# Performance work log

Measured on AMD Instinct MI355X. Metric: run time of the kernel, lower is better.

## Reference

```python
import jax, jax.numpy as jnp
import numpy as np

CONF_T = 0.6   # default conf_threshold
IOU_T = 0.5    # default iou_threshold
ALPHA = 0.25
GAMMA = 2.0


def _nms_np(boxes, scores, iou_t):
    """Greedy NMS (torchvision semantics: keep while IoU <= iou_t), returns kept indices
    into `boxes`, sorted by decreasing score. Pure numpy; data-dependent output size."""
    order = np.argsort(-scores, kind="stable")
    b = boxes[order]
    x1, y1, x2, y2 = b[:, 0], b[:, 1], b[:, 2], b[:, 3]
    areas = (x2 - x1) * (y2 - y1)
    M = b.shape[0]
    suppressed = np.zeros(M, dtype=bool)
    keep = []
    for i in range(M):
        if suppressed[i]:
            continue
        keep.append(order[i])
        if i + 1 >= M:
            break
        xx1 = np.maximum(x1[i], x1[i + 1:]); yy1 = np.maximum(y1[i], y1[i + 1:])
        xx2 = np.minimum(x2[i], x2[i + 1:]); yy2 = np.minimum(y2[i], y2[i + 1:])
        inter = np.clip(xx2 - xx1, 0, None) * np.clip(yy2 - yy1, 0, None)
        iou = inter / (areas[i] + areas[i + 1:] - inter)
        suppressed[i + 1:] |= iou > iou_t
    return np.asarray(keep, dtype=np.int64)


def _select_indices(loc, conf):
    """Concrete (non-traced) confidence filtering + NMS; index selection is
    non-differentiable in the original torch code as well."""
    conf_np = np.asarray(conf)
    if conf_np.ndim == 3:
        conf_np = conf_np[0]                      # conf.squeeze(0)
    scores = conf_np.max(axis=1)                  # conf.max(dim=1)
    filt_idx = np.nonzero(scores > CONF_T)[0]     # mask filter
    boxes = np.asarray(loc)[0, filt_idx]          # loc[:, mask, :].squeeze(0)
    nms_score = conf_np[filt_idx, 0]              # score = filtered_conf[:, 0]
    nms_keep = _nms_np(boxes, nms_score, IOU_T)
    return filt_idx, nms_keep


def _smooth_l1_sum(pred, target):
    # SmoothL1Loss(beta=1.0, reduction='sum'); target (k,4) broadcasts against
    # pred (k,C,4) exactly as torch does (requires C == k).
    d = jnp.abs(pred - target)
    return jnp.sum(jnp.where(d < 1.0, 0.5 * d * d, d - 0.5))


def _loss(loc, conf, target_boxes, target_labels_f, filt_idx, nms_keep, k):
    conf2 = conf[0] if conf.ndim == 3 else conf   # (N,C)
    floc = loc[0, filt_idx]                       # (M,4) filtered boxes
    fconf = conf2[filt_idx]                       # (M,C)
    mloc = floc[nms_keep]                         # (P,4) NMS-kept boxes
    mconf = fconf[nms_keep]                       # (P,C)
    # torch.topk(matched_conf, k, dim=0): per-class column top-k
    vals, idx = jax.lax.top_k(mconf.T, k)         # (C,k) each
    vals, idx = vals.T, idx.T                     # (k,C)
    conf_bin = (vals[:, 0] > 0.5).astype(jnp.float32)   # (k,) hard 0/1 "logits"
    pred_box = mloc[idx]                          # (k,C,4) gather, as matched_loc[indices,:]
    loc_loss = _smooth_l1_sum(pred_box, target_boxes)
    # F.cross_entropy with 1-D input and float target => soft-label CE (scalar)
    ce = -jnp.sum(target_labels_f * jax.nn.log_softmax(conf_bin))
    p_t = jnp.exp(-ce)
    conf_loss = ALPHA * (1.0 - p_t) ** GAMMA * ce
    num_pos = jnp.asarray(nms_keep.shape[0], dtype=jnp.float32)
    return (loc_loss + conf_loss) / num_pos


def setup_inputs() -> dict:
    key = jax.random.key(0)
    k0, k1, k2, k3 = jax.random.split(key, 4)
    N, C, K = 8192, 20, 20
    return {
        "loc": jax.random.uniform(k0, (1, N, 4), dtype=jnp.float32),
        "conf": jax.random.uniform(k1, (1, N, C), dtype=jnp.float32),
        "target_boxes": jax.random.uniform(k2, (K, 4), dtype=jnp.float32),
        "target_labels": jax.random.randint(k3, (K,), 0, C).astype(jnp.int64),
    }


def reference(loc, conf, target_boxes, target_labels):
    filt_idx, nms_keep = _select_indices(loc, conf)
    if filt_idx.size == 0 or nms_keep.size == 0:
        return jnp.float32(0.001)
    k = int(target_labels.shape[0])
    return _loss(loc, conf, target_boxes,
                 target_labels.astype(jnp.float32),
                 jnp.asarray(filt_idx), jnp.asarray(nms_keep), k)
```

## Files before the change

### kernel.cpp

```cpp
#include <hip/hip_runtime.h>
#include <stdint.h>
#include <stddef.h>


#define NCAP 8192
#define WROW (NCAP / 64)

typedef unsigned long long u64;

constexpr size_t OFF_CNT   = 0;
constexpr size_t OFF_KEYS  = 256;
constexpr size_t OFF_SX1   = OFF_KEYS + 8ull * NCAP;
constexpr size_t OFF_SY1   = OFF_SX1 + 4ull * NCAP;
constexpr size_t OFF_SX2   = OFF_SY1 + 4ull * NCAP;
constexpr size_t OFF_SY2   = OFF_SX2 + 4ull * NCAP;
constexpr size_t OFF_AREA  = OFF_SY2 + 4ull * NCAP;
constexpr size_t OFF_SORIG = OFF_AREA + 4ull * NCAP;
constexpr size_t OFF_KEEPS = OFF_SORIG + 4ull * NCAP;
constexpr size_t OFF_KORIG = OFF_KEEPS + 4ull * NCAP;
constexpr size_t OFF_TOPV  = OFF_KORIG + 4ull * NCAP;
constexpr size_t OFF_TOPI  = OFF_TOPV + 4096;
constexpr size_t OFF_DIAG2 = OFF_TOPI + 4096;
constexpr size_t OFF_MASK  = OFF_DIAG2 + 16ull * NCAP;
constexpr size_t WS_NEED_MASK = OFF_MASK + 8ull * NCAP * WROW;

__device__ __forceinline__ void barrier_nodrain() {
  asm volatile("s_waitcnt lgkmcnt(0)" ::: "memory");
  __builtin_amdgcn_s_barrier();
  asm volatile("" ::: "memory");
}

template <int CTRL, int RMASK>
__device__ __forceinline__ unsigned or_dpp_step(unsigned x) {
  return x | (unsigned)__builtin_amdgcn_update_dpp(0, (int)x, CTRL, RMASK, 0xf, true);
}
__device__ __forceinline__ u64 wave_or64(u64 x) {
  unsigned lo = (unsigned)x, hi = (unsigned)(x >> 32);
  lo = or_dpp_step<0x111, 0xf>(lo); hi = or_dpp_step<0x111, 0xf>(hi);
  lo = or_dpp_step<0x112, 0xf>(lo); hi = or_dpp_step<0x112, 0xf>(hi);
  lo = or_dpp_step<0x114, 0xf>(lo); hi = or_dpp_step<0x114, 0xf>(hi);
  lo = or_dpp_step<0x118, 0xf>(lo); hi = or_dpp_step<0x118, 0xf>(hi);
  lo = or_dpp_step<0x142, 0xa>(lo); hi = or_dpp_step<0x142, 0xa>(hi);
  lo = or_dpp_step<0x143, 0xc>(lo); hi = or_dpp_step<0x143, 0xc>(hi);
  lo = (unsigned)__builtin_amdgcn_readlane((int)lo, 63);
  hi = (unsigned)__builtin_amdgcn_readlane((int)hi, 63);
  return ((u64)hi << 32) | lo;
}

#define SS1(M)                                                              \
  { int tt = base + (M) * 64 + l;                                           \
    u64 a = e[M];                                                           \
    unsigned slo = __shfl_xor((unsigned)a, (int)jj);                        \
    unsigned shi = __shfl_xor((unsigned)(a >> 32), (int)jj);                \
    u64 b = ((u64)shi << 32) | slo;                                         \
    bool up = ((tt & bk) == 0);                                             \
    bool lowr = ((l & (int)jj) == 0);                                       \
    bool tmin = (up == lowr);                                               \
    bool agtb = (a > b);                                                    \
    e[M] = (tmin == agtb) ? b : a; }

#define SSTEP() { SS1(0) SS1(1) SS1(2) SS1(3) SS1(4) SS1(5) SS1(6) SS1(7) }

#define CSW(A, B)                                                           \
  { int tt = base + (A) * 64 + l;                                           \
    bool up = ((tt & bk) == 0);                                             \
    u64 xa = e[A], xb = e[B];                                               \
    bool sw = up ? (xa > xb) : (xa < xb);                                   \
    e[A] = sw ? xb : xa; e[B] = sw ? xa : xb; }

#define RSTEP4() { CSW(0,4) CSW(1,5) CSW(2,6) CSW(3,7) }
#define RSTEP2() { CSW(0,2) CSW(1,3) CSW(4,6) CSW(5,7) }
#define RSTEP1() { CSW(0,1) CSW(2,3) CSW(4,5) CSW(6,7) }

__global__ __launch_bounds__(64) void k_psort(
    const float* __restrict__ conf, int N, int C,
    u64* __restrict__ keys) {
  const int l = threadIdx.x;
  const int base = blockIdx.x * 512;
  const bool vec4 = ((C & 3) == 0);
  u64 e[8];
#pragma unroll
  for (int m = 0; m < 8; ++m) {
    int row = base + m * 64 + l;
    u64 key;
    if (row < N) {
      const float* cr = conf + (size_t)row * C;
      float mx, c0;
      if (vec4) {
        const float4* cr4 = (const float4*)cr;
        float4 q = cr4[0];
        c0 = q.x;
        mx = fmaxf(fmaxf(q.x, q.y), fmaxf(q.z, q.w));
        for (int k = 1; k < (C >> 2); ++k) {
          float4 p = cr4[k];
          mx = fmaxf(mx, fmaxf(fmaxf(p.x, p.y), fmaxf(p.z, p.w)));
        }
      } else {
        c0 = cr[0];
        mx = c0;
        for (int c = 1; c < C; ++c) mx = fmaxf(mx, cr[c]);
      }
      unsigned int k32;
      if (mx > 0.6f) {
        union { float f; unsigned int u; } s; s.f = c0;
        unsigned int u = s.u;
        u = (u & 0x80000000u) ? ~u : (u | 0x80000000u);
        k32 = ~u;
        if (k32 == 0xFFFFFFFFu) k32 = 0xFFFFFFFEu;
      } else {
        k32 = 0xFFFFFFFFu;
      }
      key = ((u64)k32 << 32) | (unsigned int)row;
    } else {
      key = ((u64)0xFFFFFFFFu << 32);
    }
    e[m] = key;
  }
  for (unsigned bk = 2; bk <= 512; bk <<= 1) {
    unsigned j = bk >> 1;
    if (j == 256) { RSTEP4(); j = 128; }
    if (j == 128) { RSTEP2(); j = 64; }
    if (j == 64)  { RSTEP1(); j = 32; }
    for (unsigned jj = j; jj >= 1; jj >>= 1) SSTEP();
  }
#pragma unroll
  for (int m = 0; m < 8; ++m) keys[base + m * 64 + l] = e[m];
}

__global__ __launch_bounds__(1024) void k_merge(
    const float* __restrict__ loc,
    u64* __restrict__ keys, unsigned int* __restrict__ cnt,
    float* __restrict__ sx1, float* __restrict__ sy1,
    float* __restrict__ sx2, float* __restrict__ sy2,
    float* __restrict__ sarea, unsigned int* __restrict__ sorig) {
  __shared__ u64 sk[NCAP];
  __shared__ int wsum[16];
  const int tid = threadIdx.x;
  const int w = tid >> 6, l = tid & 63;
  const int base = w * 512;
  u64 e[8];
#pragma unroll
  for (int m = 0; m < 8; ++m) e[m] = keys[base + m * 64 + l];

  for (unsigned bk = 1024; bk <= NCAP; bk <<= 1) {
    unsigned j = bk >> 1;
    {
#pragma unroll
      for (int m = 0; m < 8; ++m) sk[base + m * 64 + l] = e[m];
      __syncthreads();
      for (unsigned j2 = bk >> 1; j2 >= 512; j2 >>= 1) {
        for (int tl = tid; tl < NCAP; tl += 1024) {
          unsigned p = (unsigned)tl ^ j2;
          if (p > (unsigned)tl) {
            bool up = ((tl & bk) == 0);
            u64 x = sk[tl], y = sk[p];
            bool sw = up ? (x > y) : (x < y);
            if (sw) { sk[tl] = y; sk[p] = x; }
          }
        }
        __syncthreads();
      }
#pragma unroll
      for (int m = 0; m < 8; ++m) e[m] = sk[base + m * 64 + l];
      __syncthreads();
      j = 256;
    }
    if (j == 256) { RSTEP4(); j = 128; }
    if (j == 128) { RSTEP2(); j = 64; }
    if (j == 64)  { RSTEP1(); j = 32; }
    for (unsigned jj = j; jj >= 1; jj >>= 1) SSTEP();
  }

  int cv = 0;
#pragma unroll
  for (int m = 0; m < 8; ++m) {
    int idx = base + m * 64 + l;
    u64 key = e[m];
    if ((key >> 32) != 0xFFFFFFFFull) ++cv;
    unsigned row = (unsigned)(key & 0xFFFFFFFFull);
    float4 b4 = *(const float4*)(loc + (size_t)row * 4);
    float x1 = b4.x, y1 = b4.y, x2 = b4.z, y2 = b4.w;
    sx1[idx] = x1; sy1[idx] = y1; sx2[idx] = x2; sy2[idx] = y2;
    sarea[idx] = (x2 - x1) * (y2 - y1);
    sorig[idx] = row;
  }
  for (int off = 32; off; off >>= 1) cv += __shfl_down(cv, off);
  if (l == 0) wsum[w] = cv;
  __syncthreads();
  if (tid == 0) {
    int s = 0;
    for (int i = 0; i < 16; ++i) s += wsum[i];
    cnt[0] = (unsigned int)s;
  }
}

__global__ __launch_bounds__(64) void k_mask(
    const float* __restrict__ sx1, const float* __restrict__ sy1,
    const float* __restrict__ sx2, const float* __restrict__ sy2,
    const float* __restrict__ sarea,
    u64* __restrict__ mask, u64* __restrict__ diagI) {
  if (blockIdx.y < (blockIdx.x & ~1u)) return;
  __shared__ float jx1[64], jy1[64], jx2[64], jy2[64], ja[64];
  int t = threadIdx.x;
  int jbase = blockIdx.y * 64;
  jx1[t] = sx1[jbase + t]; jy1[t] = sy1[jbase + t];
  jx2[t] = sx2[jbase + t]; jy2[t] = sy2[jbase + t];
  ja[t]  = sarea[jbase + t];
  __syncthreads();
  int i = blockIdx.x * 64 + t;
  float xi1 = sx1[i], yi1 = sy1[i], xi2 = sx2[i], yi2 = sy2[i], ai = sarea[i];
  u64 bits = 0ULL;
#pragma unroll 8
  for (int jj = 0; jj < 64; ++jj) {
    float xx1 = fmaxf(xi1, jx1[jj]);
    float yy1 = fmaxf(yi1, jy1[jj]);
    float xx2 = fminf(xi2, jx2[jj]);
    float yy2 = fminf(yi2, jy2[jj]);
    float w = fmaxf(xx2 - xx1, 0.0f);
    float h = fmaxf(yy2 - yy1, 0.0f);
    float inter = w * h;
    float den = ai + ja[jj] - inter;
    float iou = inter / den;
    if (iou > 0.5f) bits |= (1ULL << jj);
  }
  mask[(size_t)i * WROW + blockIdx.y] = bits;
  if ((blockIdx.y >> 1) == (blockIdx.x >> 1))
    diagI[((size_t)i << 1) + (blockIdx.y & 1)] = bits;
}

__global__ __launch_bounds__(1024) void k_scan(
    const u64* __restrict__ mask,
    const u64* __restrict__ diagIg,
    unsigned int* __restrict__ cnt,
    unsigned int* __restrict__ keeps) {
  __shared__ __align__(16) u64 ldsDiag[2 * NCAP];
  __shared__ __align__(16) u64 rem[WROW];
  __shared__ u64 ldsKA, ldsKB;
  __shared__ int ldsKb;
  const int tid = threadIdx.x;
  const int F = (int)cnt[0];
  const int nch = (F + 127) >> 7;
  const ulonglong2* __restrict__ m2 = (const ulonglong2*)mask;

  for (int i = tid; i < 2 * NCAP; i += 1024) ldsDiag[i] = diagIg[i];
  for (int w = tid; w < WROW; w += 1024) rem[w] = 0;

  const int p0 = tid & 63;
  const int g0 = tid >> 6;
  int K = 0;
  __syncthreads();

  for (int H = 0; H < nch; ++H) {
    const size_t gb = (size_t)H * 8192;
    const int base = H << 7;
    const bool ld = (p0 > H);
    ulonglong2 v0 = {0,0}, v1 = {0,0}, v2 = {0,0}, v3 = {0,0},
               v4 = {0,0}, v5 = {0,0}, v6 = {0,0}, v7 = {0,0};
    if (ld) {
      v0 = m2[gb + tid];
      v1 = m2[gb + tid + 1024];
      v2 = m2[gb + tid + 2048];
      v3 = m2[gb + tid + 3072];
      v4 = m2[gb + tid + 4096];
      v5 = m2[gb + tid + 5120];
      v6 = m2[gb + tid + 6144];
      v7 = m2[gb + tid + 7168];
    }
    barrier_nodrain();

    if (tid < 64) {
      ulonglong2 dAB = *(const ulonglong2*)&ldsDiag[(size_t)(base + tid) << 1];
      u64 DA = dAB.x, AB = dAB.y;
      u64 DB = ldsDiag[(((size_t)(base + 64 + tid)) << 1) + 1];
      ulonglong2 supP = *(const ulonglong2*)&rem[2 * H];
      u64 sup0 = supP.x, supB0 = supP.y;

      int remrows = F - base;
      u64 validA = (remrows >= 64) ? ~0ull : ((1ull << remrows) - 1ull);
      int r2 = remrows - 64;
      u64 validB = (r2 >= 64) ? ~0ull : ((r2 <= 0) ? 0ull : ((1ull << r2) - 1ull));

      u64 DfwdA = (tid < 63) ? (DA & (~0ull << (tid + 1))) : 0ull;
      u64 undec = validA & ~sup0;
      u64 dmask = ((undec >> tid) & 1ull) ? DfwdA : 0ull;
      u64 vuln = wave_or64(dmask);
      u64 dang = __ballot(dmask != 0ull);
      u64 involved = (dang | vuln) & undec;
      u64 keepA = undec & ~involved;
      u64 und2 = involved;
      {
        unsigned Flo = (unsigned)DfwdA, Fhi = (unsigned)(DfwdA >> 32);
        while (und2) {
          int rr = __builtin_ctzll(und2);
          keepA |= 1ull << rr;
          unsigned dlo = __builtin_amdgcn_readlane(Flo, rr);
          unsigned dhi = __builtin_amdgcn_readlane(Fhi, rr);
          und2 &= ~((((u64)dhi << 32) | (u64)dlo) | (1ull << rr));
        }
      }

      u64 abm = ((keepA >> tid) & 1ull) ? AB : 0ull;
      u64 supB = supB0 | wave_or64(abm);
      u64 DfwdB = (tid < 63) ? (DB & (~0ull << (tid + 1))) : 0ull;
      u64 undecB = validB & ~supB;
      u64 dmaskB = ((undecB >> tid) & 1ull) ? DfwdB : 0ull;
      u64 vulnB = wave_or64(dmaskB);
      u64 dangB = __ballot(dmaskB != 0ull);
      u64 involvedB = (dangB | vulnB) & undecB;
      u64 keepB = undecB & ~involvedB;
      u64 und2B = involvedB;
      {
        unsigned Flo = (unsigned)DfwdB, Fhi = (unsigned)(DfwdB >> 32);
        while (und2B) {
          int rr = __builtin_ctzll(und2B);
          keepB |= 1ull << rr;
          unsigned dlo = __builtin_amdgcn_readlane(Flo, rr);
          unsigned dhi = __builtin_amdgcn_readlane(Fhi, rr);
          und2B &= ~((((u64)dhi << 32) | (u64)dlo) | (1ull << rr));
        }
      }

      if (tid == 0) { ldsKA = keepA; ldsKB = keepB; ldsKb = K; }
      K += __popcll(keepA) + __popcll(keepB);
    }
    barrier_nodrain();

    const u64 keepA = ldsKA, keepB = ldsKB;

    if (g0 == 1) {
      const int l = p0;
      const int Kb = ldsKb;
      int pcA = __popcll(keepA);
      unsigned kloA = (unsigned)keepA, khiA = (unsigned)(keepA >> 32);
      int preA = __builtin_amdgcn_mbcnt_hi(khiA, __builtin_amdgcn_mbcnt_lo(kloA, 0));
      if ((keepA >> l) & 1ull) keeps[Kb + preA] = (unsigned)(base + l);
      unsigned kloB = (unsigned)keepB, khiB = (unsigned)(keepB >> 32);
      int preB = __builtin_amdgcn_mbcnt_hi(khiB, __builtin_amdgcn_mbcnt_lo(kloB, 0));
      if ((keepB >> l) & 1ull) keeps[Kb + pcA + preB] = (unsigned)(base + 64 + l);
    }

    if (ld && (keepA | keepB)) {
      u64 ax = 0, ay = 0;
      if ((keepA >> g0) & 1ull)        { ax |= v0.x; ay |= v0.y; }
      if ((keepA >> (g0+16)) & 1ull)   { ax |= v1.x; ay |= v1.y; }
      if ((keepA >> (g0+32)) & 1ull)   { ax |= v2.x; ay |= v2.y; }
      if ((keepA >> (g0+48)) & 1ull)   { ax |= v3.x; ay |= v3.y; }
      if ((keepB >> g0) & 1ull)        { ax |= v4.x; ay |= v4.y; }
      if ((keepB >> (g0+16)) & 1ull)   { ax |= v5.x; ay |= v5.y; }
      if ((keepB >> (g0+32)) & 1ull)   { ax |= v6.x; ay |= v6.y; }
      if ((keepB >> (g0+48)) & 1ull)   { ax |= v7.x; ay |= v7.y; }
      const int w0 = 2 * p0;
      if (ax) atomicOr(&rem[w0], ax);
      if (ay) atomicOr(&rem[w0 + 1], ay);
    }
  }
  if (tid == 0) cnt[1] = (unsigned int)K;
}

__global__ __launch_bounds__(256) void k_scan_nomask(
    const float* __restrict__ sx1, const float* __restrict__ sy1,
    const float* __restrict__ sx2, const float* __restrict__ sy2,
    const float* __restrict__ sarea,
    unsigned int* __restrict__ cnt,
    unsigned int* __restrict__ keeps) {
  __shared__ unsigned char sup[NCAP];
  __shared__ int sK;
  int tid = threadIdx.x;
  int F = (int)cnt[0];
  for (int j = tid; j < NCAP; j += 256) sup[j] = 0;
  if (tid == 0) sK = 0;
  __syncthreads();
  for (int i = 0; i < F; ++i) {
    if (!sup[i]) {
      if (tid == 0) keeps[sK++] = (unsigned int)i;
      float xi1 = sx1[i], yi1 = sy1[i], xi2 = sx2[i], yi2 = sy2[i], ai = sarea[i];
      for (int j = i + 1 + tid; j < F; j += 256) {
        if (sup[j]) continue;
        float xx1 = fmaxf(xi1, sx1[j]);
        float yy1 = fmaxf(yi1, sy1[j]);
        float xx2 = fminf(xi2, sx2[j]);
        float yy2 = fminf(yi2, sy2[j]);
        float w = fmaxf(xx2 - xx1, 0.0f);
        float h = fmaxf(yy2 - yy1, 0.0f);
        float inter = w * h;
        float iou = inter / (ai + sarea[j] - inter);
        if (iou > 0.5f) sup[j] = 1;
      }
    }
    __syncthreads();
  }
  if (tid == 0) cnt[1] = (unsigned int)sK;
}

__global__ __launch_bounds__(1024) void k_topk(
    const float* __restrict__ conf,
    const unsigned int* __restrict__ sorig,
    const unsigned int* __restrict__ keeps,
    const unsigned int* __restrict__ cnt,
    int C, int KT,
    float* __restrict__ topv, int* __restrict__ topi) {
  __shared__ float wlv[16];
  __shared__ int wli[16];
  __shared__ float ldsWv;
  __shared__ int ldsWj;
  const int tid = threadIdx.x;
  const int lane = tid & 63;
  const int wv_ = tid >> 6;
  const int c = blockIdx.x;
  const int M = (int)cnt[1];

  const float NEG = -3.402823466e+38f;
  float v[8];
#pragma unroll
  for (int k = 0; k < 8; ++k) {
    int j = tid + (k << 10);
    v[k] = (j < M) ? conf[(size_t)sorig[keeps[j]] * C + c] : NEG;
  }
  float bv = NEG; int bk_ = -1;
#pragma unroll
  for (int k = 0; k < 8; ++k)
    if (v[k] > bv) { bv = v[k]; bk_ = k; }
  int bj = (bk_ >= 0) ? (tid + (bk_ << 10)) : 0x7FFFFFFF;
  if (bv == NEG) bj = 0x7FFFFFFF;

  for (int t = 0; t < KT; ++t) {
    float rv = bv; int rj = bj;
#pragma unroll
    for (int off = 32; off; off >>= 1) {
      float v2 = __shfl_down(rv, off);
      int   j2 = __shfl_down(rj, off);
      if (v2 > rv || (v2 == rv && j2 < rj)) { rv = v2; rj = j2; }
    }
    if (lane == 0) { wlv[wv_] = rv; wli[wv_] = rj; }
    __syncthreads();
    if (wv_ == 0) {
      float fv = (lane < 16) ? wlv[lane] : NEG;
      int   fj = (lane < 16) ? wli[lane] : 0x7FFFFFFF;
#pragma unroll
      for (int off = 32; off; off >>= 1) {
        float v2 = __shfl_down(fv, off);
        int   j2 = __shfl_down(fj, off);
        if (v2 > fv || (v2 == fv && j2 < fj)) { fv = v2; fj = j2; }
      }
      if (lane == 0) {
        ldsWv = fv; ldsWj = fj;
        topv[c * KT + t] = fv;
        topi[c * KT + t] = (fj == 0x7FFFFFFF) ? 0 : fj;
      }
    }
    __syncthreads();
    const int wj = ldsWj;
    if (wj != 0x7FFFFFFF && (wj & 1023) == tid) {
      int kk = wj >> 10;
#pragma unroll
      for (int k = 0; k < 8; ++k)
        if (k == kk) v[k] = NEG;
      bv = NEG; bk_ = -1;
#pragma unroll
      for (int k = 0; k < 8; ++k)
        if (v[k] > bv) { bv = v[k]; bk_ = k; }
      bj = (bk_ >= 0) ? (tid + (bk_ << 10)) : 0x7FFFFFFF;
      if (bv == NEG) bj = 0x7FFFFFFF;
    }
  }
}

__global__ __launch_bounds__(256) void k_loss(
    const float* __restrict__ loc, const float* __restrict__ tb,
    const int* __restrict__ labels,
    const unsigned int* __restrict__ sorig,
    const unsigned int* __restrict__ keeps,
    const float* __restrict__ topv, const int* __restrict__ topi,
    const unsigned int* __restrict__ cnt, int C, int KT,
    float* __restrict__ out) {
  __shared__ float red[256];
  int tid = threadIdx.x;
  int F = (int)cnt[0];
  int M = (int)cnt[1];
  if (F == 0 || M == 0) {
    if (tid == 0) out[0] = 0.001f;
    return;
  }
  int total = KT * C * 4;
  float part = 0.0f;
  for (int e = tid; e < total; e += 256) {
    int d = e & 3;
    int q = e >> 2;
    int c = q % C;
    int i = q / C;
    int j = topi[c * KT + i];
    unsigned int orow = sorig[keeps[j]];
    float pred = loc[(size_t)orow * 4 + d];
    float tg = tb[c * 4 + d];
    float dd = fabsf(pred - tg);
    part += (dd < 1.0f) ? (0.5f * dd * dd) : (dd - 0.5f);
  }
  red[tid] = part;
  __syncthreads();
  for (int s = 128; s > 0; s >>= 1) {
    if (tid < s) red[tid] += red[tid + s];
    __syncthreads();
  }
  if (tid == 0) {
    float loc_loss = red[0];
    float mx = -3.402823466e+38f;
    for (int i = 0; i < KT; ++i) {
      float x = (topv[i] > 0.5f) ? 1.0f : 0.0f;
      mx = fmaxf(mx, x);
    }
    float ssum = 0.0f;
    for (int i = 0; i < KT; ++i) {
      float x = (topv[i] > 0.5f) ? 1.0f : 0.0f;
      ssum += expf(x - mx);
    }
    float lse = mx + logf(ssum);
    float ce = 0.0f;
    for (int i = 0; i < KT; ++i) {
      float x = (topv[i] > 0.5f) ? 1.0f : 0.0f;
      ce += (float)labels[i] * (x - lse);
    }
    ce = -ce;
    float pt = expf(-ce);
    float om = 1.0f - pt;
    float conf_loss = 0.25f * om * om * ce;
    out[0] = (loc_loss + conf_loss) / (float)M;
  }
}


extern "C" void kernel_launch(void* const* d_in, const int* in_sizes, int n_in,
                              void* d_out, int out_size, void* d_ws, size_t ws_size,
                              hipStream_t stream) {
  (void)n_in; (void)out_size;
  const float* loc    = (const float*)d_in[0];
  const float* conf   = (const float*)d_in[1];
  const float* tb     = (const float*)d_in[2];
  const int*   labels = (const int*)d_in[3];
  float* out = (float*)d_out;

  int N = in_sizes[0] / 4;
  if (N > NCAP) N = NCAP;
  int C  = (N > 0) ? (in_sizes[1] / N) : 20;
  int KT = in_sizes[3];

  char* ws = (char*)d_ws;
  unsigned int* cnt   = (unsigned int*)(ws + OFF_CNT);
  u64*          keys  = (u64*)(ws + OFF_KEYS);
  float*        sx1   = (float*)(ws + OFF_SX1);
  float*        sy1   = (float*)(ws + OFF_SY1);
  float*        sx2   = (float*)(ws + OFF_SX2);
  float*        sy2   = (float*)(ws + OFF_SY2);
  float*        sarea = (float*)(ws + OFF_AREA);
  unsigned int* sorig = (unsigned int*)(ws + OFF_SORIG);
  unsigned int* keeps = (unsigned int*)(ws + OFF_KEEPS);
  float*        topv  = (float*)(ws + OFF_TOPV);
  int*          topi  = (int*)(ws + OFF_TOPI);
  u64*          diagI = (u64*)(ws + OFF_DIAG2);
  u64*          mask  = (u64*)(ws + OFF_MASK);

  bool use_mask = (ws_size >= WS_NEED_MASK);

  k_psort<<<16, 64, 0, stream>>>(conf, N, C, keys);
  k_merge<<<1, 1024, 0, stream>>>(loc, keys, cnt,
                                  sx1, sy1, sx2, sy2, sarea, sorig);
  if (use_mask) {
    k_mask<<<dim3(WROW, WROW), 64, 0, stream>>>(sx1, sy1, sx2, sy2, sarea,
                                                mask, diagI);
    k_scan<<<1, 1024, 0, stream>>>(mask, diagI, cnt, keeps);
  } else {
    k_scan_nomask<<<1, 256, 0, stream>>>(sx1, sy1, sx2, sy2, sarea, cnt, keeps);
  }
  k_topk<<<C, 1024, 0, stream>>>(conf, sorig, keeps, cnt, C, KT, topv, topi);
  k_loss<<<1, 256, 0, stream>>>(loc, tb, labels, sorig, keeps, topv, topi, cnt, C, KT, out);
}
```

Baseline: 300.0 us.

## Prefetch next mask chunk in scan and fuse loss into top-k kernel

The NMS scan kernel now issues the global loads for chunk H+1 before processing chunk H, using double-buffered registers so memory latency overlaps the serial per-chunk decision work. Separately, the loss kernel is folded into the top-k kernel through a last-block-done pattern: each block atomically increments a counter (reset in the merge kernel), and the final block computes the loss. This removes one kernel launch at the cost of extra register pressure in the scan and an atomic plus threadfence in top-k.

```diff
diff --git a/kernel.cpp b/kernel.cpp
--- a/kernel.cpp
+++ b/kernel.cpp
@@ -191,6 +191,7 @@
     int s = 0;
     for (int i = 0; i < 16; ++i) s += wsum[i];
     cnt[0] = (unsigned int)s;
+    cnt[2] = 0u;
   }
 }
 
@@ -248,23 +249,36 @@
   const int p0 = tid & 63;
   const int g0 = tid >> 6;
   int K = 0;
+
+  ulonglong2 v0 = {0,0}, v1 = {0,0}, v2 = {0,0}, v3 = {0,0},
+             v4 = {0,0}, v5 = {0,0}, v6 = {0,0}, v7 = {0,0};
+  if (nch > 0 && p0 > 0) {
+    v0 = m2[tid];
+    v1 = m2[tid + 1024];
+    v2 = m2[tid + 2048];
+    v3 = m2[tid + 3072];
+    v4 = m2[tid + 4096];
+    v5 = m2[tid + 5120];
+    v6 = m2[tid + 6144];
+    v7 = m2[tid + 7168];
+  }
   __syncthreads();
 
   for (int H = 0; H < nch; ++H) {
-    const size_t gb = (size_t)H * 8192;
     const int base = H << 7;
     const bool ld = (p0 > H);
-    ulonglong2 v0 = {0,0}, v1 = {0,0}, v2 = {0,0}, v3 = {0,0},
-               v4 = {0,0}, v5 = {0,0}, v6 = {0,0}, v7 = {0,0};
-    if (ld) {
-      v0 = m2[gb + tid];
-      v1 = m2[gb + tid + 1024];
-      v2 = m2[gb + tid + 2048];
-      v3 = m2[gb + tid + 3072];
-      v4 = m2[gb + tid + 4096];
-      v5 = m2[gb + tid + 5120];
-      v6 = m2[gb + tid + 6144];
-      v7 = m2[gb + tid + 7168];
+    ulonglong2 n0 = {0,0}, n1 = {0,0}, n2 = {0,0}, n3 = {0,0},
+               n4 = {0,0}, n5 = {0,0}, n6 = {0,0}, n7 = {0,0};
+    if (H + 1 < nch && p0 > H + 1) {
+      const size_t gbn = (size_t)(H + 1) * 8192;
+      n0 = m2[gbn + tid];
+      n1 = m2[gbn + tid + 1024];
+      n2 = m2[gbn + tid + 2048];
+      n3 = m2[gbn + tid + 3072];
+      n4 = m2[gbn + tid + 4096];
+      n5 = m2[gbn + tid + 5120];
+      n6 = m2[gbn + tid + 6144];
+      n7 = m2[gbn + tid + 7168];
     }
     barrier_nodrain();
 
@@ -353,6 +367,8 @@
       if (ax) atomicOr(&rem[w0], ax);
       if (ay) atomicOr(&rem[w0 + 1], ay);
     }
+    v0 = n0; v1 = n1; v2 = n2; v3 = n3;
+    v4 = n4; v5 = n5; v6 = n6; v7 = n7;
   }
   if (tid == 0) cnt[1] = (unsigned int)K;
 }
@@ -394,15 +410,20 @@
 
 __global__ __launch_bounds__(1024) void k_topk(
     const float* __restrict__ conf,
+    const float* __restrict__ loc, const float* __restrict__ tb,
+    const int* __restrict__ labels,
     const unsigned int* __restrict__ sorig,
     const unsigned int* __restrict__ keeps,
-    const unsigned int* __restrict__ cnt,
+    unsigned int* __restrict__ cnt,
     int C, int KT,
-    float* __restrict__ topv, int* __restrict__ topi) {
+    float* __restrict__ topv, int* __restrict__ topi,
+    float* __restrict__ out) {
   __shared__ float wlv[16];
   __shared__ int wli[16];
   __shared__ float ldsWv;
   __shared__ int ldsWj;
+  __shared__ unsigned int sLast;
+  __shared__ float red[1024];
   const int tid = threadIdx.x;
   const int lane = tid & 63;
   const int wv_ = tid >> 6;
@@ -463,41 +484,38 @@
       if (bv == NEG) bj = 0x7FFFFFFF;
     }
   }
-}
-
-__global__ __launch_bounds__(256) void k_loss(
-    const float* __restrict__ loc, const float* __restrict__ tb,
-    const int* __restrict__ labels,
-    const unsigned int* __restrict__ sorig,
-    const unsigned int* __restrict__ keeps,
-    const float* __restrict__ topv, const int* __restrict__ topi,
-    const unsigned int* __restrict__ cnt, int C, int KT,
-    float* __restrict__ out) {
-  __shared__ float red[256];
-  int tid = threadIdx.x;
-  int F = (int)cnt[0];
-  int M = (int)cnt[1];
+
+  if (tid == 0) {
+    __threadfence();
+    unsigned int prev = atomicAdd(&cnt[2], 1u);
+    sLast = (prev == (unsigned int)(gridDim.x - 1)) ? 1u : 0u;
+  }
+  __syncthreads();
+  if (sLast == 0u) return;
+  __threadfence();
+
+  const int F = (int)cnt[0];
   if (F == 0 || M == 0) {
     if (tid == 0) out[0] = 0.001f;
     return;
   }
   int total = KT * C * 4;
   float part = 0.0f;
-  for (int e = tid; e < total; e += 256) {
+  for (int e = tid; e < total; e += 1024) {
     int d = e & 3;
     int q = e >> 2;
-    int c = q % C;
+    int cc = q % C;
     int i = q / C;
-    int j = topi[c * KT + i];
+    int j = topi[cc * KT + i];
     unsigned int orow = sorig[keeps[j]];
     float pred = loc[(size_t)orow * 4 + d];
-    float tg = tb[c * 4 + d];
+    float tg = tb[cc * 4 + d];
     float dd = fabsf(pred - tg);
     part += (dd < 1.0f) ? (0.5f * dd * dd) : (dd - 0.5f);
   }
   red[tid] = part;
   __syncthreads();
-  for (int s = 128; s > 0; s >>= 1) {
+  for (int s = 512; s > 0; s >>= 1) {
     if (tid < s) red[tid] += red[tid + s];
     __syncthreads();
   }
@@ -570,6 +588,6 @@
   } else {
     k_scan_nomask<<<1, 256, 0, stream>>>(sx1, sy1, sx2, sy2, sarea, cnt, keeps);
   }
-  k_topk<<<C, 1024, 0, stream>>>(conf, sorig, keeps, cnt, C, KT, topv, topi);
-  k_loss<<<1, 256, 0, stream>>>(loc, tb, labels, sorig, keeps, topv, topi, cnt, C, KT, out);
-}
+  k_topk<<<C, 1024, 0, stream>>>(conf, loc, tb, labels, sorig, keeps, cnt,
+                                 C, KT, topv, topi, out);
+}
```

New measurement: 303.8 us. Within noise of the previous version (+1.3%).
